# Performance work log

Hardware: AMD Instinct MI355X
Metric: run time of the kernel (lower is better)

The kernel has to match this reference:

```python
import jax, jax.numpy as jnp
import numpy as np
from jax import lax

DIM = 384
NUM_HEADS = 8
KV_NUM_HEADS = 2
REP = NUM_HEADS // KV_NUM_HEADS  # 4
KV_DIM = DIM * 2 // REP          # 192
EPS_LN = 1e-5
EPS_NORM = 1e-12


def _layernorm_channel(x, w, b):
    # WithBias LayerNorm over channel dim of NCHW tensor (matches to_3d -> LN(c) -> to_4d)
    mu = jnp.mean(x, axis=1, keepdims=True)
    var = jnp.var(x, axis=1, keepdims=True)
    return (x - mu) / jnp.sqrt(var + EPS_LN) * w[None, :, None, None] + b[None, :, None, None]


def _conv1x1(x, w):
    # w: [out, in] ; x: [b, in, h, w]
    return jnp.einsum('oi,bihw->bohw', w, x)


def _dwconv3x3(x, w):
    # depthwise 3x3, padding=1; w: [C, 1, 3, 3]
    C = x.shape[1]
    return lax.conv_general_dilated(
        x, w, window_strides=(1, 1), padding=((1, 1), (1, 1)),
        feature_group_count=C,
        dimension_numbers=('NCHW', 'OIHW', 'NCHW'))


def _l2norm(x):
    n = jnp.linalg.norm(x, axis=-1, keepdims=True)
    return x / jnp.maximum(n, EPS_NORM)


def setup_inputs() -> dict:
    key = jax.random.key(0)
    ks = jax.random.split(key, 8)
    b, h, w = 8, 128, 128
    scale1 = 1.0 / np.sqrt(DIM)
    return {
        'q': jax.random.normal(ks[0], (b, DIM, h, w), dtype=jnp.float32),
        'k': jax.random.normal(ks[1], (b, DIM, h, w), dtype=jnp.float32),
        'w_q': jax.random.normal(ks[2], (DIM, DIM), dtype=jnp.float32) * scale1,
        'w_kv': jax.random.normal(ks[3], (KV_DIM, DIM), dtype=jnp.float32) * scale1,
        'w_q_dw': jax.random.normal(ks[4], (DIM, 1, 3, 3), dtype=jnp.float32) * (1.0 / 3.0),
        'w_kv_dw': jax.random.normal(ks[5], (KV_DIM, 1, 3, 3), dtype=jnp.float32) * (1.0 / 3.0),
        'w_out': jax.random.normal(ks[6], (DIM, DIM), dtype=jnp.float32) * scale1,
        'temperature': jnp.ones((NUM_HEADS, 1, 1), dtype=jnp.float32),
        'lnq_w': jnp.ones((DIM,), dtype=jnp.float32),
        'lnq_b': jnp.zeros((DIM,), dtype=jnp.float32),
        'lnk_w': jnp.ones((DIM,), dtype=jnp.float32),
        'lnk_b': jnp.zeros((DIM,), dtype=jnp.float32),
    }


def reference(q, k, w_q, w_kv, w_q_dw, w_kv_dw, w_out, temperature,
              lnq_w, lnq_b, lnk_w, lnk_b):
    b, c, h, w = q.shape
    hw = h * w
    qn = _layernorm_channel(q, lnq_w, lnq_b)
    kn = _layernorm_channel(k, lnk_w, lnk_b)
    qp = _dwconv3x3(_conv1x1(qn, w_q), w_q_dw)          # [b, dim, h, w]
    kv = _dwconv3x3(_conv1x1(kn, w_kv), w_kv_dw)        # [b, 2*dim/rep, h, w]
    kk, vv = jnp.split(kv, 2, axis=1)                   # each [b, dim/rep, h, w]
    # reshape to heads: channel-attention layout [b, head, c_head, hw]
    qh = qp.reshape(b, NUM_HEADS, DIM // NUM_HEADS, hw)
    kh = kk.reshape(b, KV_NUM_HEADS, DIM // NUM_HEADS, hw)
    vh = vv.reshape(b, KV_NUM_HEADS, DIM // NUM_HEADS, hw)
    # GQA repeat kv heads (repeat_interleave on head dim)
    kh = jnp.repeat(kh, REP, axis=1)
    vh = jnp.repeat(vh, REP, axis=1)
    qh = _l2norm(qh)
    kh = _l2norm(kh)
    attn = jnp.einsum('bhck,bhdk->bhcd', qh, kh) * temperature[None]
    attn = jax.nn.softmax(attn, axis=-1)
    out = jnp.einsum('bhcd,bhdk->bhck', attn, vh)       # [b, head, c_head, hw]
    out = out.reshape(b, DIM, h, w)
    return _conv1x1(out, w_out)
```

## Files before the change

### kernel.cpp

```cpp
#include <hip/hip_runtime.h>
#include <math.h>


typedef unsigned short u16;
typedef unsigned int u32;
typedef short s16x8 __attribute__((ext_vector_type(8)));
typedef float f32x4 __attribute__((ext_vector_type(4)));

#define HW 16384
#define NB 8
#define CDIM 384
#define KVC 192

__device__ __forceinline__ float b2f(u16 u) {
  return __uint_as_float(((u32)u) << 16);
}
__device__ __forceinline__ u16 f2b(float f) {
  u32 u = __float_as_uint(f);
  u += 0x7fffu + ((u >> 16) & 1u);
  return (u16)(u >> 16);
}
__device__ __forceinline__ int swz(int r) {
  return (r & 3) ^ ((r >> 2) & 3) ^ ((r >> 4) & 3);
}
__device__ __forceinline__ void gll16(const void* g, void* l) {
  __builtin_amdgcn_global_load_lds(
      (const __attribute__((address_space(1))) u32*)g,
      (__attribute__((address_space(3))) u32*)l, 16, 0, 0);
}

__global__ void k0_prep(const float* __restrict__ wq, const float* __restrict__ wkv,
                        const float* __restrict__ wo,
                        const float* __restrict__ lnqw, const float* __restrict__ lnqb,
                        const float* __restrict__ lnkw, const float* __restrict__ lnkb,
                        u16* __restrict__ wqp, float* __restrict__ rwsQ, float* __restrict__ biasQ,
                        u16* __restrict__ wkvp, float* __restrict__ rwsKV, float* __restrict__ biasKV,
                        u16* __restrict__ wop) {
  int r = blockIdx.x * 256 + threadIdx.x;
  if (r < 384) {
    float rs = 0.f, bs = 0.f;
    for (int i = 0; i < 384; ++i) {
      float wp = wq[r * 384 + i] * lnqw[i];
      u16 h = f2b(wp);
      rs += b2f(h);
      bs += wq[r * 384 + i] * lnqb[i];
      wqp[r * 384 + i] = h;
    }
    rwsQ[r] = rs; biasQ[r] = bs;
  } else if (r < 640) {
    int o = r - 384;
    if (o < 192) {
      float rs = 0.f, bs = 0.f;
      for (int i = 0; i < 384; ++i) {
        float wp = wkv[o * 384 + i] * lnkw[i];
        u16 h = f2b(wp);
        rs += b2f(h);
        bs += wkv[o * 384 + i] * lnkb[i];
        wkvp[o * 384 + i] = h;
      }
      rwsKV[o] = rs; biasKV[o] = bs;
    } else {
      for (int i = 0; i < 384; ++i) wkvp[o * 384 + i] = 0;
      rwsKV[o] = 0.f; biasKV[o] = 0.f;
    }
  } else {
    int o = r - 640;
    for (int i = 0; i < 384; ++i) wop[o * 384 + i] = f2b(wo[o * 384 + i]);
  }
}

template <int MODE>
__global__ __launch_bounds__(256, 4) void gemm_fused(const u16* __restrict__ A,
                                                     const void* __restrict__ Bsrc,
                                                     const float* __restrict__ rowsum,
                                                     const float* __restrict__ bias,
                                                     void* __restrict__ outv, int M) {
  __shared__ u16 tA[2][128 * 32];
  __shared__ u16 tB[2][64 * 32];
  __shared__ float2 sred[4][64];
  __shared__ float muL[64], sdL[64];

  const int b = blockIdx.z, ot = blockIdx.y, pt = blockIdx.x;
  const int tid = threadIdx.x;
  const int w = tid >> 6, l = tid & 63;
  const int wm = w >> 1, wn = w & 1, lr = l & 15, lg = l >> 4;

  f32x4 acc[4][2] = {};

  const int rA0 = tid >> 2, cA0 = tid & 3;
  const int rA1 = (256 + tid) >> 2, cA1 = tid & 3;
  const u16* aS0 = A + (size_t)(ot * 128 + rA0) * 384 + (cA0 ^ swz(rA0)) * 8;
  const u16* aS1 = A + (size_t)(ot * 128 + rA1) * 384 + (cA1 ^ swz(rA1)) * 8;
  const int aDst0 = (w * 64) * 8;
  const int aDst1 = (256 + w * 64) * 8;

  const float* Bf = (const float*)Bsrc;
  const u16* Bh = (const u16*)Bsrc;
  const size_t fbase = (size_t)b * CDIM * HW + (size_t)pt * 64 + l;
  const int bWrChunk = w ^ swz(l);
  const int rB = tid >> 2, cB = tid & 3;
  const u16* bS = Bh + ((size_t)(b * HW + pt * 64 + rB)) * 384 + (cB ^ swz(rB)) * 8;
  const int bDst = (w * 64) * 8;

  float pv[8];
  float sum = 0.f, sq = 0.f;

  auto stageA = [&](int ks, int buf) {
    gll16(aS0 + ks * 32, &tA[buf][aDst0]);
    gll16(aS1 + ks * 32, &tA[buf][aDst1]);
  };
  auto loadB = [&](int ks) {
    if (MODE == 0) {
#pragma unroll
      for (int e = 0; e < 8; ++e)
        pv[e] = Bf[fbase + (size_t)(ks * 32 + w * 8 + e) * HW];
    } else {
      gll16(bS + ks * 32, &tB[0][0] + (size_t)0);
    }
  };
  auto stageB1 = [&](int ks, int buf) {
    gll16(bS + ks * 32, &tB[buf][bDst]);
  };
  auto storeB0 = [&](int buf) {
    u32 pk[4];
#pragma unroll
    for (int e = 0; e < 8; e += 2) {
      float v0 = pv[e], v1 = pv[e + 1];
      sum += v0 + v1;
      sq += v0 * v0 + v1 * v1;
      pk[e >> 1] = (u32)f2b(v0) | ((u32)f2b(v1) << 16);
    }
    *(uint4*)&tB[buf][l * 32 + bWrChunk * 8] = make_uint4(pk[0], pk[1], pk[2], pk[3]);
  };

  stageA(0, 0);
  if (MODE == 0) { loadB(0); storeB0(0); }
  else { stageB1(0, 0); }
  __syncthreads();

  int cur = 0;
  for (int ks = 0; ks < 12; ++ks) {
    if (ks < 11) {
      stageA(ks + 1, cur ^ 1);
      if (MODE == 0) loadB(ks + 1);
      else stageB1(ks + 1, cur ^ 1);
    }

    s16x8 a[4], bb[2];
#pragma unroll
    for (int mf = 0; mf < 4; ++mf) {
      int row = wm * 64 + mf * 16 + lr;
      a[mf] = *(const s16x8*)&tA[cur][row * 32 + (lg ^ swz(row)) * 8];
    }
#pragma unroll
    for (int nf = 0; nf < 2; ++nf) {
      int row = wn * 32 + nf * 16 + lr;
      bb[nf] = *(const s16x8*)&tB[cur][row * 32 + (lg ^ swz(row)) * 8];
    }
#pragma unroll
    for (int mf = 0; mf < 4; ++mf)
#pragma unroll
      for (int nf = 0; nf < 2; ++nf)
        acc[mf][nf] = __builtin_amdgcn_mfma_f32_16x16x32_bf16(a[mf], bb[nf], acc[mf][nf], 0, 0, 0);

    if (ks < 11 && MODE == 0) storeB0(cur ^ 1);
    __syncthreads();
    cur ^= 1;
  }

  if (MODE == 0) {
    sred[w][l] = make_float2(sum, sq);
    __syncthreads();
    if (tid < 64) {
      float s = 0.f, q2 = 0.f;
#pragma unroll
      for (int g = 0; g < 4; ++g) { s += sred[g][tid].x; q2 += sred[g][tid].y; }
      float mn = s * (1.f / 384.f);
      float var = q2 * (1.f / 384.f) - mn * mn;
      muL[tid] = mn;
      sdL[tid] = rsqrtf(var + 1e-5f);
    }
    __syncthreads();
  }

#pragma unroll
  for (int nf = 0; nf < 2; ++nf) {
    int row = wn * 32 + nf * 16 + lr;
    int p = pt * 64 + row;
    float m_ = 0.f, s_ = 0.f;
    if (MODE == 0) { m_ = muL[row]; s_ = sdL[row]; }
#pragma unroll
    for (int mf = 0; mf < 4; ++mf) {
#pragma unroll
      for (int r = 0; r < 4; ++r) {
        int o = ot * 128 + wm * 64 + mf * 16 + lg * 4 + r;
        if (MODE == 0) {
          if (o < M) {
            float v = s_ * (acc[mf][nf][r] - m_ * rowsum[o]) + bias[o];
            ((u16*)outv)[((size_t)(b * M + o)) * HW + p] = f2b(v);
          }
        } else {
          ((float*)outv)[((size_t)(b * CDIM + o)) * HW + p] = acc[mf][nf][r];
        }
      }
    }
  }
}

__global__ __launch_bounds__(256) void k4_dw(const u16* __restrict__ qp, const u16* __restrict__ kvp,
                                             const float* __restrict__ wqdw, const float* __restrict__ wkvdw,
                                             u16* __restrict__ qd, u16* __restrict__ kvd,
                                             float* __restrict__ rnq, float* __restrict__ rnk) {
  __shared__ u16 plane[16384];
  __shared__ float red[256];

  int c = blockIdx.x, b = blockIdx.y;
  int tid = threadIdx.x;
  const u16* in; u16* outb; const float* wp; int C;
  int isQ = (c < 384), cc = isQ ? c : c - 384;
  if (isQ) { in = qp; outb = qd; wp = wqdw + cc * 9; C = CDIM; }
  else     { in = kvp; outb = kvd; wp = wkvdw + cc * 9; C = KVC; }
  size_t base = ((size_t)(b * C + cc)) * HW;

  float w[9];
#pragma unroll
  for (int j = 0; j < 9; ++j) w[j] = wp[j];

  const uint4* gsrc = (const uint4*)(in + base);
  uint4* lplane = (uint4*)plane;
#pragma unroll
  for (int i = 0; i < 8; ++i) lplane[tid + i * 256] = gsrc[tid + i * 256];
  __syncthreads();

  uint4* gdst = (uint4*)(outb + base);
  float ns = 0.f;
#pragma unroll
  for (int it = 0; it < 8; ++it) {
    int idx = tid + it * 256;
    int y = idx >> 4, ox = idx & 15;
    int x0 = ox * 8;

    float r[3][10];
#pragma unroll
    for (int rr = 0; rr < 3; ++rr) {
      int yy = y + rr - 1;
      if ((unsigned)yy < 128u) {
        int rbase = yy * 128 + x0;
        r[rr][0] = (x0 > 0) ? b2f(plane[rbase - 1]) : 0.f;
        uint4 v = *(const uint4*)&plane[rbase];
        u32 ws[4] = {v.x, v.y, v.z, v.w};
#pragma unroll
        for (int j = 0; j < 4; ++j) {
          r[rr][1 + 2 * j] = b2f((u16)(ws[j] & 0xffff));
          r[rr][2 + 2 * j] = b2f((u16)(ws[j] >> 16));
        }
        r[rr][9] = (x0 < 120) ? b2f(plane[rbase + 8]) : 0.f;
      } else {
#pragma unroll
        for (int j = 0; j < 10; ++j) r[rr][j] = 0.f;
      }
    }

    u32 packed[4];
#pragma unroll
    for (int j = 0; j < 8; ++j) {
      float a = 0.f;
#pragma unroll
      for (int rr = 0; rr < 3; ++rr)
#pragma unroll
        for (int dx = 0; dx < 3; ++dx)
          a += w[rr * 3 + dx] * r[rr][j + dx];
      u16 h = f2b(a);
      float hv = b2f(h);
      ns += hv * hv;
      if (j & 1) packed[j >> 1] |= ((u32)h) << 16; else packed[j >> 1] = (u32)h;
    }
    gdst[idx] = make_uint4(packed[0], packed[1], packed[2], packed[3]);
  }

  red[tid] = ns;
  __syncthreads();
  for (int st = 128; st > 0; st >>= 1) {
    if (tid < st) red[tid] += red[tid + st];
    __syncthreads();
  }
  if (tid == 0) {
    float n = sqrtf(red[0]);
    float inv = 1.f / fmaxf(n, 1e-12f);
    if (isQ) rnq[b * 384 + cc] = inv;
    else if (cc < 96) rnk[b * 96 + cc] = inv;
  }
}

__global__ void k5b_vt(const u16* __restrict__ kvd, u16* __restrict__ vt) {
  int p = blockIdx.x * 256 + threadIdx.x;
  int b = blockIdx.y;
  size_t sb = ((size_t)(b * KVC + 96)) * HW + p;
  uint4* dv = (uint4*)vt + ((size_t)(b * HW + p)) * 12;
  for (int j8 = 0; j8 < 12; ++j8) {
    u32 w[4];
#pragma unroll
    for (int j = 0; j < 8; ++j) {
      u16 h = kvd[sb + (size_t)(j8 * 8 + j) * HW];
      if (j & 1) w[j >> 1] |= ((u32)h) << 16; else w[j >> 1] = (u32)h;
    }
    dv[j8] = make_uint4(w[0], w[1], w[2], w[3]);
  }
}

__global__ __launch_bounds__(256) void k6_qk(const u16* __restrict__ qd,
                                             const u16* __restrict__ kvd,
                                             float* __restrict__ spart) {
  int kc = blockIdx.x, h = blockIdx.y, b = blockIdx.z;
  int tid = threadIdx.x;
  int w = tid >> 6, l = tid & 63, lr = l & 15, lg = l >> 4;
  int g = h >> 2;
  int p0 = kc * 1024 + w * 256;

  f32x4 acc[3][3] = {};
  size_t qbase = ((size_t)(b * CDIM + h * 48 + lr)) * HW;
  size_t kbase = ((size_t)(b * KVC + g * 48 + lr)) * HW;

  for (int ks = 0; ks < 8; ++ks) {
    int pp = p0 + ks * 32 + lg * 8;
    s16x8 a[3], bb[3];
#pragma unroll
    for (int mi = 0; mi < 3; ++mi) a[mi] = *(const s16x8*)(qd + qbase + (size_t)mi * 16 * HW + pp);
#pragma unroll
    for (int ni = 0; ni < 3; ++ni) bb[ni] = *(const s16x8*)(kvd + kbase + (size_t)ni * 16 * HW + pp);
#pragma unroll
    for (int mi = 0; mi < 3; ++mi)
#pragma unroll
      for (int ni = 0; ni < 3; ++ni)
        acc[mi][ni] = __builtin_amdgcn_mfma_f32_16x16x32_bf16(a[mi], bb[ni], acc[mi][ni], 0, 0, 0);
  }

  size_t sb = ((size_t)((((b * 8 + h) * 16) + kc) * 4 + w)) * 2304;
#pragma unroll
  for (int mi = 0; mi < 3; ++mi)
#pragma unroll
    for (int ni = 0; ni < 3; ++ni)
#pragma unroll
      for (int r = 0; r < 4; ++r) {
        int c = mi * 16 + lg * 4 + r, d = ni * 16 + lr;
        spart[sb + c * 48 + d] = acc[mi][ni][r];
      }
}

__global__ void k7_sm(const float* __restrict__ spart, const float* __restrict__ temp,
                      const float* __restrict__ rnq, const float* __restrict__ rnk,
                      u16* __restrict__ ptil) {
  int h = blockIdx.x, b = blockIdx.y, tid = threadIdx.x;
  int g = h >> 2;
  __shared__ float S[2304];
  size_t base = ((size_t)((b * 8 + h) * 64)) * 2304;
  for (int e = tid; e < 2304; e += 64) {
    float s = 0.f;
    for (int j = 0; j < 64; ++j) s += spart[base + (size_t)j * 2304 + e];
    S[e] = s;
  }
  __syncthreads();
  if (tid < 48) {
    int c = tid;
    float sq = temp[h] * rnq[b * 384 + h * 48 + c];
    float mx = -1e30f;
    for (int d = 0; d < 48; ++d) {
      float v = S[c * 48 + d] * sq * rnk[b * 96 + g * 48 + d];
      mx = fmaxf(mx, v);
    }
    float sum = 0.f;
    for (int d = 0; d < 48; ++d) {
      float v = S[c * 48 + d] * sq * rnk[b * 96 + g * 48 + d];
      sum += __expf(v - mx);
    }
    float inv = 1.f / sum;
    u16* row = ptil + ((size_t)(b * 384 + h * 48 + c)) * 96;
    for (int dk = 0; dk < 96; ++dk) {
      int d = dk - g * 48;
      float pv = 0.f;
      if (d >= 0 && d < 48) {
        float v = S[c * 48 + d] * sq * rnk[b * 96 + g * 48 + d];
        pv = __expf(v - mx) * inv;
      }
      row[dk] = f2b(pv);
    }
  }
}

__global__ __launch_bounds__(512) void k8_pv(const u16* __restrict__ vt,
                                             const u16* __restrict__ ptil,
                                             u16* __restrict__ yt) {
  int ptb = blockIdx.x, b = blockIdx.y;
  int tid = threadIdx.x;
  int w = tid >> 6, l = tid & 63, lr = l & 15, lg = l >> 4;
  int wm = w >> 2, wn = w & 3;

  f32x4 acc[4][6] = {};
  size_t arow0 = ((size_t)(b * HW + ptb * 128 + wm * 64 + lr)) * 96;
  size_t brow0 = ((size_t)(b * CDIM + wn * 96 + lr)) * 96;

  for (int ks = 0; ks < 3; ++ks) {
    int ko = ks * 32 + lg * 8;
    s16x8 a[4], bb[6];
#pragma unroll
    for (int mf = 0; mf < 4; ++mf) a[mf] = *(const s16x8*)(vt + arow0 + (size_t)mf * 16 * 96 + ko);
#pragma unroll
    for (int nf = 0; nf < 6; ++nf) bb[nf] = *(const s16x8*)(ptil + brow0 + (size_t)nf * 16 * 96 + ko);
#pragma unroll
    for (int mf = 0; mf < 4; ++mf)
#pragma unroll
      for (int nf = 0; nf < 6; ++nf)
        acc[mf][nf] = __builtin_amdgcn_mfma_f32_16x16x32_bf16(a[mf], bb[nf], acc[mf][nf], 0, 0, 0);
  }

#pragma unroll
  for (int mf = 0; mf < 4; ++mf)
#pragma unroll
    for (int nf = 0; nf < 6; ++nf)
#pragma unroll
      for (int r = 0; r < 4; ++r) {
        int p = ptb * 128 + wm * 64 + mf * 16 + lg * 4 + r;
        int c = wn * 96 + nf * 16 + lr;
        yt[((size_t)(b * HW + p)) * 384 + c] = f2b(acc[mf][nf][r]);
      }
}

extern "C" void kernel_launch(void* const* d_in, const int* in_sizes, int n_in,
                              void* d_out, int out_size, void* d_ws, size_t ws_size,
                              hipStream_t stream) {
  const float* q    = (const float*)d_in[0];
  const float* k    = (const float*)d_in[1];
  const float* w_q  = (const float*)d_in[2];
  const float* w_kv = (const float*)d_in[3];
  const float* w_qd = (const float*)d_in[4];
  const float* w_kd = (const float*)d_in[5];
  const float* w_o  = (const float*)d_in[6];
  const float* temp = (const float*)d_in[7];
  const float* lnqw = (const float*)d_in[8];
  const float* lnqb = (const float*)d_in[9];
  const float* lnkw = (const float*)d_in[10];
  const float* lnkb = (const float*)d_in[11];
  float* out = (float*)d_out;

  char* ws = (char*)d_ws;
  size_t off = 0;
  auto alloc = [&](size_t bytes) -> void* {
    void* p = ws + off;
    off += (bytes + 255) & ~(size_t)255;
    return p;
  };

  u16*   wqp   = (u16*)alloc(384 * 384 * 2);
  float* rwsQ  = (float*)alloc(384 * 4);
  float* biasQ = (float*)alloc(384 * 4);
  u16*   wkvp  = (u16*)alloc(256 * 384 * 2);
  float* rwsKV = (float*)alloc(256 * 4);
  float* biasKV= (float*)alloc(256 * 4);
  u16*   wop   = (u16*)alloc(384 * 384 * 2);
  u16*   qp    = (u16*)alloc((size_t)NB * CDIM * HW * 2);
  u16*   kvp   = (u16*)alloc((size_t)NB * KVC * HW * 2);
  u16*   qd    = (u16*)alloc((size_t)NB * CDIM * HW * 2);
  u16*   kvd   = (u16*)alloc((size_t)NB * KVC * HW * 2);
  u16*   vt    = (u16*)alloc((size_t)NB * HW * 96 * 2);
  float* spart = (float*)alloc((size_t)4096 * 2304 * 4);
  u16*   ptil  = (u16*)alloc((size_t)NB * CDIM * 96 * 2);
  float* rnq   = (float*)alloc((size_t)NB * 384 * 4);
  float* rnk   = (float*)alloc((size_t)NB * 96 * 4);

  u16* yt = qp;

  k0_prep<<<4, 256, 0, stream>>>(w_q, w_kv, w_o, lnqw, lnqb, lnkw, lnkb,
                                 wqp, rwsQ, biasQ, wkvp, rwsKV, biasKV, wop);

  gemm_fused<0><<<dim3(256, 3, NB), 256, 0, stream>>>(wqp, q, rwsQ, biasQ, qp, 384);
  gemm_fused<0><<<dim3(256, 2, NB), 256, 0, stream>>>(wkvp, k, rwsKV, biasKV, kvp, 192);

  k4_dw<<<dim3(576, NB), 256, 0, stream>>>(qp, kvp, w_qd, w_kd, qd, kvd, rnq, rnk);

  k5b_vt<<<dim3(64, NB), 256, 0, stream>>>(kvd, vt);

  k6_qk<<<dim3(16, 8, NB), 256, 0, stream>>>(qd, kvd, spart);
  k7_sm<<<dim3(8, NB), 64, 0, stream>>>(spart, temp, rnq, rnk, ptil);

  k8_pv<<<dim3(128, NB), 512, 0, stream>>>(vt, ptil, yt);

  gemm_fused<1><<<dim3(256, 3, NB), 256, 0, stream>>>(wop, yt, nullptr, nullptr, out, 384);
}
```

Baseline: 616.5 us.

## Triple-buffer GEMM LDS tiles with prefetch distance two and manual waitcnts

Moves the fused GEMM from a double-buffered to a triple-buffered LDS pipeline. Global loads run two k-steps ahead, and fp32 B operands are held in two register buffers. The full __syncthreads is replaced with explicit s_waitcnt vmcnt counts plus s_barrier, so in-flight loads can overlap MFMA work. This costs more LDS per block, which may reduce occupancy, and the hand-counted vmcnt values are fragile if the compiler reorders loads.

```diff
diff --git a/kernel.cpp b/kernel.cpp
--- a/kernel.cpp
+++ b/kernel.cpp
@@ -75,8 +75,8 @@
                                                      const float* __restrict__ rowsum,
                                                      const float* __restrict__ bias,
                                                      void* __restrict__ outv, int M) {
-  __shared__ u16 tA[2][128 * 32];
-  __shared__ u16 tB[2][64 * 32];
+  __shared__ u16 tA[3][128 * 32];
+  __shared__ u16 tB[3][64 * 32];
   __shared__ float2 sred[4][64];
   __shared__ float muL[64], sdL[64];
 
@@ -88,9 +88,9 @@
   f32x4 acc[4][2] = {};
 
   const int rA0 = tid >> 2, cA0 = tid & 3;
-  const int rA1 = (256 + tid) >> 2, cA1 = tid & 3;
+  const int rA1 = 64 + rA0;
   const u16* aS0 = A + (size_t)(ot * 128 + rA0) * 384 + (cA0 ^ swz(rA0)) * 8;
-  const u16* aS1 = A + (size_t)(ot * 128 + rA1) * 384 + (cA1 ^ swz(rA1)) * 8;
+  const u16* aS1 = A + (size_t)(ot * 128 + rA1) * 384 + (cA0 ^ swz(rA1)) * 8;
   const int aDst0 = (w * 64) * 8;
   const int aDst1 = (256 + w * 64) * 8;
 
@@ -98,34 +98,30 @@
   const u16* Bh = (const u16*)Bsrc;
   const size_t fbase = (size_t)b * CDIM * HW + (size_t)pt * 64 + l;
   const int bWrChunk = w ^ swz(l);
-  const int rB = tid >> 2, cB = tid & 3;
-  const u16* bS = Bh + ((size_t)(b * HW + pt * 64 + rB)) * 384 + (cB ^ swz(rB)) * 8;
+  const int rB = tid >> 2;
+  const u16* bS = Bh + ((size_t)(b * HW + pt * 64 + rB)) * 384 + ((tid & 3) ^ swz(rB)) * 8;
   const int bDst = (w * 64) * 8;
 
-  float pv[8];
+  float pvbuf[2][8];
   float sum = 0.f, sq = 0.f;
 
   auto stageA = [&](int ks, int buf) {
     gll16(aS0 + ks * 32, &tA[buf][aDst0]);
     gll16(aS1 + ks * 32, &tA[buf][aDst1]);
   };
-  auto loadB = [&](int ks) {
-    if (MODE == 0) {
-#pragma unroll
-      for (int e = 0; e < 8; ++e)
-        pv[e] = Bf[fbase + (size_t)(ks * 32 + w * 8 + e) * HW];
-    } else {
-      gll16(bS + ks * 32, &tB[0][0] + (size_t)0);
-    }
-  };
   auto stageB1 = [&](int ks, int buf) {
     gll16(bS + ks * 32, &tB[buf][bDst]);
   };
-  auto storeB0 = [&](int buf) {
+  auto loadB0 = [&](int ks, float* pvv) {
+#pragma unroll
+    for (int e = 0; e < 8; ++e)
+      pvv[e] = Bf[fbase + (size_t)(ks * 32 + w * 8 + e) * HW];
+  };
+  auto storeB0 = [&](const float* pvv, int buf) {
     u32 pk[4];
 #pragma unroll
     for (int e = 0; e < 8; e += 2) {
-      float v0 = pv[e], v1 = pv[e + 1];
+      float v0 = pvv[e], v1 = pvv[e + 1];
       sum += v0 + v1;
       sq += v0 * v0 + v1 * v1;
       pk[e >> 1] = (u32)f2b(v0) | ((u32)f2b(v1) << 16);
@@ -133,29 +129,40 @@
     *(uint4*)&tB[buf][l * 32 + bWrChunk * 8] = make_uint4(pk[0], pk[1], pk[2], pk[3]);
   };
 
-  stageA(0, 0);
-  if (MODE == 0) { loadB(0); storeB0(0); }
-  else { stageB1(0, 0); }
-  __syncthreads();
-
-  int cur = 0;
+  if (MODE == 0) {
+    stageA(0, 0); loadB0(0, pvbuf[0]);
+    stageA(1, 1); loadB0(1, pvbuf[1]);
+    asm volatile("s_waitcnt vmcnt(10)" ::: "memory");
+    storeB0(pvbuf[0], 0);
+    asm volatile("s_waitcnt lgkmcnt(0)" ::: "memory");
+  } else {
+    stageA(0, 0); stageB1(0, 0);
+    stageA(1, 1); stageB1(1, 1);
+    asm volatile("s_waitcnt vmcnt(3)" ::: "memory");
+  }
+  __builtin_amdgcn_s_barrier();
+
+#pragma unroll
   for (int ks = 0; ks < 12; ++ks) {
-    if (ks < 11) {
-      stageA(ks + 1, cur ^ 1);
-      if (MODE == 0) loadB(ks + 1);
-      else stageB1(ks + 1, cur ^ 1);
+    const int cb = ks % 3;
+    const int nb_ = (ks + 2) % 3;
+
+    if (ks < 10) {
+      stageA(ks + 2, nb_);
+      if (MODE == 0) loadB0(ks + 2, pvbuf[ks & 1]);
+      else stageB1(ks + 2, nb_);
     }
 
     s16x8 a[4], bb[2];
 #pragma unroll
     for (int mf = 0; mf < 4; ++mf) {
       int row = wm * 64 + mf * 16 + lr;
-      a[mf] = *(const s16x8*)&tA[cur][row * 32 + (lg ^ swz(row)) * 8];
+      a[mf] = *(const s16x8*)&tA[cb][row * 32 + ((lg ^ swz(row)) * 8)];
     }
 #pragma unroll
     for (int nf = 0; nf < 2; ++nf) {
       int row = wn * 32 + nf * 16 + lr;
-      bb[nf] = *(const s16x8*)&tB[cur][row * 32 + (lg ^ swz(row)) * 8];
+      bb[nf] = *(const s16x8*)&tB[cb][row * 32 + ((lg ^ swz(row)) * 8)];
     }
 #pragma unroll
     for (int mf = 0; mf < 4; ++mf)
@@ -163,9 +170,16 @@
       for (int nf = 0; nf < 2; ++nf)
         acc[mf][nf] = __builtin_amdgcn_mfma_f32_16x16x32_bf16(a[mf], bb[nf], acc[mf][nf], 0, 0, 0);
 
-    if (ks < 11 && MODE == 0) storeB0(cur ^ 1);
-    __syncthreads();
-    cur ^= 1;
+    if (MODE == 0 && ks < 11) storeB0(pvbuf[(ks + 1) & 1], (ks + 1) % 3);
+
+    if (MODE == 0) {
+      if (ks < 10)      asm volatile("s_waitcnt vmcnt(10) lgkmcnt(0)" ::: "memory");
+      else              asm volatile("s_waitcnt vmcnt(0) lgkmcnt(0)" ::: "memory");
+    } else {
+      if (ks < 10)      asm volatile("s_waitcnt vmcnt(3) lgkmcnt(0)" ::: "memory");
+      else              asm volatile("s_waitcnt vmcnt(0) lgkmcnt(0)" ::: "memory");
+    }
+    __builtin_amdgcn_s_barrier();
   }
 
   if (MODE == 0) {
```

New measurement: 613.8 us. Within noise of the previous version (-0.4%).

## Enlarge GEMM pixel tile to 256 with 512-thread blocks and float4 B loads

Applied to the files above, without the earlier changes.

The fused 1x1-conv GEMMs now use 512-thread blocks covering 128 output channels by 256 pixels instead of 64, with each wave computing a 64x64 sub-tile (4x4 MFMA fragments). In the LayerNorm-fused mode, the fp32 input is read as float4 along pixels and stored transposed into a padded (stride 36) LDS tile, replacing the XOR swizzle. Per-pixel sum and sum-of-squares are reduced across 8 waves. The aim is more MFMA work per LDS read and wider global loads, at the cost of more registers and LDS and fewer blocks in the grid.

```diff
diff --git a/kernel.cpp b/kernel.cpp
--- a/kernel.cpp
+++ b/kernel.cpp
@@ -70,111 +70,111 @@
 }
 
 template <int MODE>
-__global__ __launch_bounds__(256, 4) void gemm_fused(const u16* __restrict__ A,
+__global__ __launch_bounds__(512, 4) void gemm_fused(const u16* __restrict__ A,
                                                      const void* __restrict__ Bsrc,
                                                      const float* __restrict__ rowsum,
                                                      const float* __restrict__ bias,
                                                      void* __restrict__ outv, int M) {
   __shared__ u16 tA[2][128 * 32];
-  __shared__ u16 tB[2][64 * 32];
-  __shared__ float2 sred[4][64];
-  __shared__ float muL[64], sdL[64];
+  __shared__ u16 tB[2][MODE == 0 ? 256 * 36 : 256 * 32];
+  __shared__ float sredS[MODE == 0 ? 8 : 1][MODE == 0 ? 256 : 1];
+  __shared__ float sredQ[MODE == 0 ? 8 : 1][MODE == 0 ? 256 : 1];
+  __shared__ float muL[MODE == 0 ? 256 : 1], sdL[MODE == 0 ? 256 : 1];
 
   const int b = blockIdx.z, ot = blockIdx.y, pt = blockIdx.x;
   const int tid = threadIdx.x;
   const int w = tid >> 6, l = tid & 63;
-  const int wm = w >> 1, wn = w & 1, lr = l & 15, lg = l >> 4;
-
-  f32x4 acc[4][2] = {};
-
-  const int rA0 = tid >> 2, cA0 = tid & 3;
-  const int rA1 = (256 + tid) >> 2, cA1 = tid & 3;
-  const u16* aS0 = A + (size_t)(ot * 128 + rA0) * 384 + (cA0 ^ swz(rA0)) * 8;
-  const u16* aS1 = A + (size_t)(ot * 128 + rA1) * 384 + (cA1 ^ swz(rA1)) * 8;
-  const int aDst0 = (w * 64) * 8;
-  const int aDst1 = (256 + w * 64) * 8;
+  const int wm = w >> 2, wn = w & 3, lr = l & 15, lg = l >> 4;
+
+  f32x4 acc[4][4] = {};
+
+  const int rA = tid >> 2, cA = tid & 3;
+  const u16* aS = A + (size_t)(ot * 128 + rA) * 384 + (cA ^ swz(rA)) * 8;
+  u16* aDst0 = &tA[0][w * 512];
+  u16* aDst1 = &tA[1][w * 512];
 
   const float* Bf = (const float*)Bsrc;
   const u16* Bh = (const u16*)Bsrc;
-  const size_t fbase = (size_t)b * CDIM * HW + (size_t)pt * 64 + l;
-  const int bWrChunk = w ^ swz(l);
-  const int rB = tid >> 2, cB = tid & 3;
-  const u16* bS = Bh + ((size_t)(b * HW + pt * 64 + rB)) * 384 + (cB ^ swz(rB)) * 8;
-  const int bDst = (w * 64) * 8;
-
-  float pv[8];
-  float sum = 0.f, sq = 0.f;
+  const size_t fbase = (size_t)b * CDIM * HW + (size_t)pt * 256 + 4 * l;
+  const int rB = tid >> 2;
+  const u16* bS0 = Bh + ((size_t)(b * HW + pt * 256 + rB)) * 384 + ((tid & 3) ^ swz(rB)) * 8;
+  const u16* bS1 = Bh + ((size_t)(b * HW + pt * 256 + 128 + rB)) * 384 + ((tid & 3) ^ swz(128 + rB)) * 8;
+
+  float4 pv[4];
+  float sum4[4] = {0.f, 0.f, 0.f, 0.f}, sq4[4] = {0.f, 0.f, 0.f, 0.f};
 
   auto stageA = [&](int ks, int buf) {
-    gll16(aS0 + ks * 32, &tA[buf][aDst0]);
-    gll16(aS1 + ks * 32, &tA[buf][aDst1]);
-  };
-  auto loadB = [&](int ks) {
-    if (MODE == 0) {
-#pragma unroll
-      for (int e = 0; e < 8; ++e)
-        pv[e] = Bf[fbase + (size_t)(ks * 32 + w * 8 + e) * HW];
-    } else {
-      gll16(bS + ks * 32, &tB[0][0] + (size_t)0);
-    }
+    gll16(aS + ks * 32, buf ? aDst1 : aDst0);
   };
   auto stageB1 = [&](int ks, int buf) {
-    gll16(bS + ks * 32, &tB[buf][bDst]);
+    gll16(bS0 + ks * 32, &tB[buf][w * 512]);
+    gll16(bS1 + ks * 32, &tB[buf][4096 + w * 512]);
+  };
+  auto loadB0 = [&](int ks) {
+#pragma unroll
+    for (int j = 0; j < 4; ++j)
+      pv[j] = *(const float4*)(Bf + fbase + (size_t)(ks * 32 + w * 4 + j) * HW);
   };
   auto storeB0 = [&](int buf) {
-    u32 pk[4];
-#pragma unroll
-    for (int e = 0; e < 8; e += 2) {
-      float v0 = pv[e], v1 = pv[e + 1];
-      sum += v0 + v1;
-      sq += v0 * v0 + v1 * v1;
-      pk[e >> 1] = (u32)f2b(v0) | ((u32)f2b(v1) << 16);
-    }
-    *(uint4*)&tB[buf][l * 32 + bWrChunk * 8] = make_uint4(pk[0], pk[1], pk[2], pk[3]);
+#pragma unroll
+    for (int i = 0; i < 4; ++i) {
+      float v0 = pv[0][i], v1 = pv[1][i], v2 = pv[2][i], v3 = pv[3][i];
+      sum4[i] += (v0 + v1) + (v2 + v3);
+      sq4[i] += (v0 * v0 + v1 * v1) + (v2 * v2 + v3 * v3);
+      u32 lo = (u32)f2b(v0) | ((u32)f2b(v1) << 16);
+      u32 hi = (u32)f2b(v2) | ((u32)f2b(v3) << 16);
+      *(uint2*)&tB[buf][(4 * l + i) * 36 + w * 4] = make_uint2(lo, hi);
+    }
   };
 
-  stageA(0, 0);
-  if (MODE == 0) { loadB(0); storeB0(0); }
-  else { stageB1(0, 0); }
+  if (MODE == 0) { loadB0(0); stageA(0, 0); storeB0(0); }
+  else { stageB1(0, 0); stageA(0, 0); }
   __syncthreads();
 
   int cur = 0;
+#pragma unroll
   for (int ks = 0; ks < 12; ++ks) {
+    const int nxt = cur ^ 1;
     if (ks < 11) {
-      stageA(ks + 1, cur ^ 1);
-      if (MODE == 0) loadB(ks + 1);
-      else stageB1(ks + 1, cur ^ 1);
-    }
-
-    s16x8 a[4], bb[2];
+      if (MODE == 0) loadB0(ks + 1);
+      stageA(ks + 1, nxt);
+      if (MODE == 1) stageB1(ks + 1, nxt);
+    }
+
+    s16x8 a[4], bb[4];
 #pragma unroll
     for (int mf = 0; mf < 4; ++mf) {
       int row = wm * 64 + mf * 16 + lr;
       a[mf] = *(const s16x8*)&tA[cur][row * 32 + (lg ^ swz(row)) * 8];
     }
 #pragma unroll
-    for (int nf = 0; nf < 2; ++nf) {
-      int row = wn * 32 + nf * 16 + lr;
-      bb[nf] = *(const s16x8*)&tB[cur][row * 32 + (lg ^ swz(row)) * 8];
+    for (int nf = 0; nf < 4; ++nf) {
+      int row = wn * 64 + nf * 16 + lr;
+      if (MODE == 0) bb[nf] = *(const s16x8*)&tB[cur][row * 36 + lg * 8];
+      else           bb[nf] = *(const s16x8*)&tB[cur][row * 32 + (lg ^ swz(row)) * 8];
     }
 #pragma unroll
     for (int mf = 0; mf < 4; ++mf)
 #pragma unroll
-      for (int nf = 0; nf < 2; ++nf)
+      for (int nf = 0; nf < 4; ++nf)
         acc[mf][nf] = __builtin_amdgcn_mfma_f32_16x16x32_bf16(a[mf], bb[nf], acc[mf][nf], 0, 0, 0);
 
-    if (ks < 11 && MODE == 0) storeB0(cur ^ 1);
+    if (MODE == 0 && ks < 11) storeB0(nxt);
     __syncthreads();
-    cur ^= 1;
+    cur = nxt;
   }
 
   if (MODE == 0) {
-    sred[w][l] = make_float2(sum, sq);
+#pragma unroll
+    for (int i = 0; i < 4; ++i) {
+      sredS[w][4 * l + i] = sum4[i];
+      sredQ[w][4 * l + i] = sq4[i];
+    }
     __syncthreads();
-    if (tid < 64) {
+    if (tid < 256) {
       float s = 0.f, q2 = 0.f;
 #pragma unroll
-      for (int g = 0; g < 4; ++g) { s += sred[g][tid].x; q2 += sred[g][tid].y; }
+      for (int g = 0; g < 8; ++g) { s += sredS[g][tid]; q2 += sredQ[g][tid]; }
       float mn = s * (1.f / 384.f);
       float var = q2 * (1.f / 384.f) - mn * mn;
       muL[tid] = mn;
@@ -184,9 +184,9 @@
   }
 
 #pragma unroll
-  for (int nf = 0; nf < 2; ++nf) {
-    int row = wn * 32 + nf * 16 + lr;
-    int p = pt * 64 + row;
+  for (int nf = 0; nf < 4; ++nf) {
+    int row = wn * 64 + nf * 16 + lr;
+    int p = pt * 256 + row;
     float m_ = 0.f, s_ = 0.f;
     if (MODE == 0) { m_ = muL[row]; s_ = sdL[row]; }
 #pragma unroll
@@ -472,8 +472,8 @@
   k0_prep<<<4, 256, 0, stream>>>(w_q, w_kv, w_o, lnqw, lnqb, lnkw, lnkb,
                                  wqp, rwsQ, biasQ, wkvp, rwsKV, biasKV, wop);
 
-  gemm_fused<0><<<dim3(256, 3, NB), 256, 0, stream>>>(wqp, q, rwsQ, biasQ, qp, 384);
-  gemm_fused<0><<<dim3(256, 2, NB), 256, 0, stream>>>(wkvp, k, rwsKV, biasKV, kvp, 192);
+  gemm_fused<0><<<dim3(64, 3, NB), 512, 0, stream>>>(wqp, q, rwsQ, biasQ, qp, 384);
+  gemm_fused<0><<<dim3(64, 2, NB), 512, 0, stream>>>(wkvp, k, rwsKV, biasKV, kvp, 192);
 
   k4_dw<<<dim3(576, NB), 256, 0, stream>>>(qp, kvp, w_qd, w_kd, qd, kvd, rnq, rnk);
 
@@ -484,5 +484,5 @@
 
   k8_pv<<<dim3(128, NB), 512, 0, stream>>>(vt, ptil, yt);
 
-  gemm_fused<1><<<dim3(256, 3, NB), 256, 0, stream>>>(wop, yt, nullptr, nullptr, out, 384);
-}
+  gemm_fused<1><<<dim3(64, 3, NB), 512, 0, stream>>>(wop, yt, nullptr, nullptr, out, 384);
+}
```

Measured after the change: 1.372 ms. 123% more time.
